# Kernel optimization log

Hardware: AMD Instinct MI355X
Metric: run time of the kernel (lower is better)

Reference implementation:

```python
import jax, jax.numpy as jnp
import numpy as np
from functools import partial

B, T, D, H, K = 4, 2048, 256, 8, 31
HD = D // H
EXP = 2  # FeedForward expansion
EPS = 1e-5


def setup_inputs() -> dict:
    key = jax.random.key(0)
    ks = iter(jax.random.split(key, 32))
    s = 0.02
    n = lambda shape: jax.random.normal(next(ks), shape, jnp.float32) * s
    ones = lambda shape: jnp.ones(shape, jnp.float32)
    zeros = lambda shape: jnp.zeros(shape, jnp.float32)
    return {
        "x": jax.random.normal(next(ks), (B, T, D), jnp.float32),
        # FF1
        "ff1_ln_g": ones((D,)), "ff1_ln_b": zeros((D,)),
        "ff1_w1": n((D, D * EXP)), "ff1_b1": zeros((D * EXP,)),
        "ff1_w2": n((D * EXP, D)), "ff1_b2": zeros((D,)),
        # MHSA
        "mhsa_ln_g": ones((D,)), "mhsa_ln_b": zeros((D,)),
        "qkv_w": n((D, 3 * D)), "qkv_b": zeros((3 * D,)),
        "out_w": n((D, D)), "out_b": zeros((D,)),
        # Conv module
        "conv_ln_g": ones((D,)), "conv_ln_b": zeros((D,)),
        "pw1_w": n((D, 2 * D)), "pw1_b": zeros((2 * D,)),
        "dw_w": n((D, 1, K)), "dw_b": zeros((D,)),
        "bn_g": ones((D,)), "bn_b": zeros((D,)),
        "pw2_w": n((D, D)), "pw2_b": zeros((D,)),
        # FF2
        "ff2_ln_g": ones((D,)), "ff2_ln_b": zeros((D,)),
        "ff2_w1": n((D, D * EXP)), "ff2_b1": zeros((D * EXP,)),
        "ff2_w2": n((D * EXP, D)), "ff2_b2": zeros((D,)),
        # Final LN
        "final_ln_g": ones((D,)), "final_ln_b": zeros((D,)),
    }


def layer_norm(x, g, b):
    mu = jnp.mean(x, axis=-1, keepdims=True)
    var = jnp.mean(jnp.square(x - mu), axis=-1, keepdims=True)
    return (x - mu) * jax.lax.rsqrt(var + EPS) * g + b


def feed_forward(x, ln_g, ln_b, w1, b1, w2, b2):
    h = layer_norm(x, ln_g, ln_b)
    h = jax.nn.silu(h @ w1 + b1)
    h = h @ w2 + b2
    return x + 0.5 * h


def mhsa(x, ln_g, ln_b, qkv_w, qkv_b, out_w, out_b):
    Bc, Tc, C = x.shape
    h = layer_norm(x, ln_g, ln_b)
    qkv = (h @ qkv_w + qkv_b).reshape(Bc, Tc, 3, H, HD)
    qkv = jnp.transpose(qkv, (2, 0, 3, 1, 4))  # [3,B,H,T,hd]
    q, k, v = qkv[0], qkv[1], qkv[2]
    attn = jnp.einsum("bhqd,bhkd->bhqk", q, k) / jnp.sqrt(jnp.float32(HD))
    attn = jax.nn.softmax(attn, axis=-1)
    out = jnp.einsum("bhqk,bhkd->bhqd", attn, v)
    out = jnp.transpose(out, (0, 2, 1, 3)).reshape(Bc, Tc, C)
    return x + (out @ out_w + out_b)


def conv_module(x, ln_g, ln_b, pw1_w, pw1_b, dw_w, dw_b, bn_g, bn_b, pw2_w, pw2_b):
    h = layer_norm(x, ln_g, ln_b)
    h = h @ pw1_w + pw1_b                      # [B,T,2D]
    a, g = jnp.split(h, 2, axis=-1)
    h = a * jax.nn.sigmoid(g)                  # GLU -> [B,T,D]
    h = jnp.transpose(h, (0, 2, 1))            # [B,D,T]
    h = jax.lax.conv_general_dilated(
        h, dw_w, window_strides=(1,), padding=[(K // 2, K // 2)],
        dimension_numbers=("NCH", "OIH", "NCH"), feature_group_count=D,
    ) + dw_b[None, :, None]
    # BatchNorm1d (training-mode batch stats, biased variance) over (B,T) per channel
    mu = jnp.mean(h, axis=(0, 2), keepdims=True)
    var = jnp.mean(jnp.square(h - mu), axis=(0, 2), keepdims=True)
    h = (h - mu) * jax.lax.rsqrt(var + EPS)
    h = h * bn_g[None, :, None] + bn_b[None, :, None]
    h = jax.nn.silu(h)
    h = jnp.transpose(h, (0, 2, 1))            # [B,T,D]
    h = h @ pw2_w + pw2_b
    return x + h


def reference(x,
              ff1_ln_g, ff1_ln_b, ff1_w1, ff1_b1, ff1_w2, ff1_b2,
              mhsa_ln_g, mhsa_ln_b, qkv_w, qkv_b, out_w, out_b,
              conv_ln_g, conv_ln_b, pw1_w, pw1_b, dw_w, dw_b, bn_g, bn_b,
              pw2_w, pw2_b,
              ff2_ln_g, ff2_ln_b, ff2_w1, ff2_b1, ff2_w2, ff2_b2,
              final_ln_g, final_ln_b):
    x = feed_forward(x, ff1_ln_g, ff1_ln_b, ff1_w1, ff1_b1, ff1_w2, ff1_b2)
    x = mhsa(x, mhsa_ln_g, mhsa_ln_b, qkv_w, qkv_b, out_w, out_b)
    x = conv_module(x, conv_ln_g, conv_ln_b, pw1_w, pw1_b, dw_w, dw_b,
                    bn_g, bn_b, pw2_w, pw2_b)
    x = feed_forward(x, ff2_ln_g, ff2_ln_b, ff2_w1, ff2_b1, ff2_w2, ff2_b2)
    return layer_norm(x, final_ln_g, final_ln_b)
```

## Files before the change

### kernel.cpp

```cpp
#include <hip/hip_runtime.h>
#include <hip/hip_bf16.h>

#define Bn 4
#define Tn 2048
#define Dn 256
#define Hn 8
#define HDn 32
#define KW 31
#define EPSV 1e-5f
#define NTOK (Bn * Tn)

typedef __attribute__((ext_vector_type(8))) short bf16x8;
typedef __attribute__((ext_vector_type(4))) float f32x4;
typedef unsigned short ushort_t;

__device__ __forceinline__ float sigmoidf_(float x) { return 1.f / (1.f + __expf(-x)); }
__device__ __forceinline__ unsigned short f2bfu(float f) {
    __hip_bfloat16 h = __float2bfloat16(f);
    unsigned short u; __builtin_memcpy(&u, &h, 2); return u;
}

template <int OUTBF>
__global__ __launch_bounds__(256) void ln_kernel(const float* __restrict__ x,
                                                 const float* __restrict__ g,
                                                 const float* __restrict__ b,
                                                 void* __restrict__ yp)
{
    const int row  = blockIdx.x * 4 + (threadIdx.x >> 6);
    const int lane = threadIdx.x & 63;
    const float* xr = x + (size_t)row * Dn + lane * 4;
    float4 v = *(const float4*)xr;
    float s = v.x + v.y + v.z + v.w;
#pragma unroll
    for (int o = 32; o > 0; o >>= 1) s += __shfl_xor(s, o, 64);
    const float mu = s * (1.f / Dn);
    const float dx = v.x - mu, dy = v.y - mu, dz = v.z - mu, dw = v.w - mu;
    float ss = dx * dx + dy * dy + dz * dz + dw * dw;
#pragma unroll
    for (int o = 32; o > 0; o >>= 1) ss += __shfl_xor(ss, o, 64);
    const float rstd = rsqrtf(ss * (1.f / Dn) + EPSV);
    const float4 gv = *(const float4*)(g + lane * 4);
    const float4 bv = *(const float4*)(b + lane * 4);
    float o0 = dx * rstd * gv.x + bv.x;
    float o1 = dy * rstd * gv.y + bv.y;
    float o2 = dz * rstd * gv.z + bv.z;
    float o3 = dw * rstd * gv.w + bv.w;
    if (OUTBF) {
        ushort4 o4;
        o4.x = f2bfu(o0); o4.y = f2bfu(o1); o4.z = f2bfu(o2); o4.w = f2bfu(o3);
        *(ushort4*)((ushort_t*)yp + (size_t)row * Dn + lane * 4) = o4;
    } else {
        float4 o4 = {o0, o1, o2, o3};
        *(float4*)((float*)yp + (size_t)row * Dn + lane * 4) = o4;
    }
}

struct WP {
    const float* s[8];
    unsigned     off[8];
    int          Kd[8];
    int          Nd[8];
};

__global__ __launch_bounds__(256) void wprep_kernel(WP p, ushort_t* __restrict__ wb)
{
    const int z = blockIdx.z;
    const int N = p.Nd[z], K = p.Kd[z];
    const int n0 = blockIdx.x * 64, k0 = blockIdx.y * 32;
    if (n0 >= N || k0 >= K) return;
    const float* src = p.s[z];
    ushort_t* dst = wb + p.off[z];
    const int nl = threadIdx.x & 63, kq = threadIdx.x >> 6;
    const int n = n0 + nl;
    const int kb = k0 + kq * 8;
    bf16x8 o;
#pragma unroll
    for (int i = 0; i < 8; ++i) o[i] = (short)f2bfu(src[(size_t)(kb + i) * N + n]);
    *(bf16x8*)(dst + (size_t)n * K + kb) = o;
}

template <int EPI, int BM>
__global__ __launch_bounds__(256) void bgemm_kernel(const ushort_t* __restrict__ A,
                                                    const ushort_t* __restrict__ Bt,
                                                    const float* __restrict__ bias,
                                                    const float* __restrict__ res,
                                                    void* __restrict__ Cp,
                                                    int N, int K, float scale)
{
    constexpr int ABLK = BM / 16;
    constexpr int AST  = ABLK / 4;
    constexpr int MT   = BM / 32;
    __shared__ ushort_t Af[ABLK][64][8];
    __shared__ ushort_t Bf[4][64][8];
    const int tid = threadIdx.x;
    const int w   = tid >> 6;
    const int l   = tid & 63;
    const int g   = l >> 4;
    const int q16 = l & 15;
    const int wm  = w >> 1;
    const int wn  = w & 1;
    const int row0 = blockIdx.x * BM;
    const int col0 = blockIdx.y * 64;
    const int sbi  = tid >> 6;

    const ushort_t* ga[AST];
#pragma unroll
    for (int i = 0; i < AST; ++i)
        ga[i] = A + (size_t)(row0 + (sbi + 4 * i) * 16 + q16) * K + g * 8;
    const ushort_t* gb = Bt + (size_t)(col0 + sbi * 16 + q16) * K + g * 8;

    f32x4 acc[MT][2];
#pragma unroll
    for (int mt = 0; mt < MT; ++mt)
#pragma unroll
        for (int nt = 0; nt < 2; ++nt) { acc[mt][nt].x = 0.f; acc[mt][nt].y = 0.f; acc[mt][nt].z = 0.f; acc[mt][nt].w = 0.f; }

    bf16x8 sa[AST], sb;
#pragma unroll
    for (int i = 0; i < AST; ++i) sa[i] = *(const bf16x8*)ga[i];
    sb = *(const bf16x8*)gb;

    const int NKT = K >> 5;
    for (int kt = 0; kt < NKT; ++kt) {
        __syncthreads();
#pragma unroll
        for (int i = 0; i < AST; ++i) *(bf16x8*)&Af[sbi + 4 * i][l][0] = sa[i];
        *(bf16x8*)&Bf[sbi][l][0] = sb;
        if (kt + 1 < NKT) {
            const int k = (kt + 1) * 32;
#pragma unroll
            for (int i = 0; i < AST; ++i) sa[i] = *(const bf16x8*)(ga[i] + k);
            sb = *(const bf16x8*)(gb + k);
        }
        __syncthreads();
        bf16x8 af[MT], bb[2];
#pragma unroll
        for (int mt = 0; mt < MT; ++mt) af[mt] = *(const bf16x8*)&Af[wm * MT + mt][l][0];
#pragma unroll
        for (int nt = 0; nt < 2; ++nt) bb[nt] = *(const bf16x8*)&Bf[wn * 2 + nt][l][0];
#pragma unroll
        for (int mt = 0; mt < MT; ++mt)
#pragma unroll
            for (int nt = 0; nt < 2; ++nt)
                acc[mt][nt] = __builtin_amdgcn_mfma_f32_16x16x32_bf16(af[mt], bb[nt], acc[mt][nt], 0, 0, 0);
    }

#pragma unroll
    for (int nt = 0; nt < 2; ++nt) {
        const int col = col0 + (wn * 2 + nt) * 16 + q16;
        const float bj = bias[col];
#pragma unroll
        for (int mt = 0; mt < MT; ++mt) {
            const int rowb = row0 + (wm * MT + mt) * 16 + g * 4;
#pragma unroll
            for (int r = 0; r < 4; ++r) {
                float v = acc[mt][nt][r] + bj;
                const size_t idx = (size_t)(rowb + r) * N + col;
                if (EPI == 1) v *= sigmoidf_(v);
                if (EPI == 0 || EPI == 1) {
                    ((ushort_t*)Cp)[idx] = f2bfu(v);
                } else if (EPI == 2) {
                    ((float*)Cp)[idx] = res[idx] + scale * v;
                } else {
                    ((float*)Cp)[idx] = v;
                }
            }
        }
    }
}

__global__ __launch_bounds__(256) void attn_mfma_kernel(const ushort_t* __restrict__ qkv,
                                                        ushort_t* __restrict__ out)
{
    __shared__ ushort_t Kl[4][64][40];
    __shared__ ushort_t Vt[4][32][72];
    __shared__ ushort_t Pl[4][16][72];

    const int tid = threadIdx.x;
    const int w   = tid >> 6;
    const int l   = tid & 63;
    const int g   = l >> 4;
    const int q16 = l & 15;
    const int b   = blockIdx.y >> 3;
    const int h   = blockIdx.y & 7;
    const int q0  = blockIdx.x * 128 + w * 32;
    const ushort_t* base = qkv + (size_t)b * Tn * 768;

    bf16x8 qf[2];
#pragma unroll
    for (int u = 0; u < 2; ++u)
        qf[u] = *(const bf16x8*)(base + (size_t)(q0 + u * 16 + q16) * 768 + h * 32 + g * 8);

    f32x4 O[2][2];
    float mrun[2][4], lrun[2][4];
#pragma unroll
    for (int u = 0; u < 2; ++u)
#pragma unroll
        for (int t = 0; t < 2; ++t) { O[u][t].x = 0.f; O[u][t].y = 0.f; O[u][t].z = 0.f; O[u][t].w = 0.f; }
#pragma unroll
    for (int u = 0; u < 2; ++u)
#pragma unroll
        for (int r = 0; r < 4; ++r) { mrun[u][r] = 0.f; lrun[u][r] = 0.f; }

    const float cs = 0.25505392367033404f;

    const ushort_t* kvp = base + (size_t)l * 768 + 256 + h * 32;
    bf16x8 nk[4], nv[4];
#pragma unroll
    for (int j = 0; j < 4; ++j) {
        nk[j] = *(const bf16x8*)(kvp + j * 8);
        nv[j] = *(const bf16x8*)(kvp + 256 + j * 8);
    }

    for (int c0 = 0; c0 < Tn; c0 += 64) {
#pragma unroll
        for (int j = 0; j < 4; ++j)
            *(bf16x8*)&Kl[w][l][j * 8] = nk[j];
#pragma unroll
        for (int j = 0; j < 4; ++j) {
            const int vcol = l ^ (16 * j);
#pragma unroll
            for (int i = 0; i < 8; ++i)
                Vt[w][j * 8 + i][vcol] = (ushort_t)nv[j][i];
        }
        if (c0 + 64 < Tn) {
            const ushort_t* np = kvp + (size_t)(c0 + 64) * 768;
#pragma unroll
            for (int j = 0; j < 4; ++j) {
                nk[j] = *(const bf16x8*)(np + j * 8);
                nv[j] = *(const bf16x8*)(np + 256 + j * 8);
            }
        }

        bf16x8 kb[4];
#pragma unroll
        for (int t = 0; t < 4; ++t)
            kb[t] = *(const bf16x8*)&Kl[w][t * 16 + q16][g * 8];
        bf16x8 vb[2][2];
#pragma unroll
        for (int ht = 0; ht < 2; ++ht) {
            const int d = ht * 16 + q16;
#pragma unroll
            for (int c = 0; c < 2; ++c)
                vb[ht][c] = *(const bf16x8*)&Vt[w][d][(c * 32 + g * 8) ^ ((d & 24) << 1)];
        }

#pragma unroll
        for (int u = 0; u < 2; ++u) {
            float p[4][4];
#pragma unroll
            for (int t = 0; t < 4; ++t) {
                f32x4 z = {0.f, 0.f, 0.f, 0.f};
                f32x4 s = __builtin_amdgcn_mfma_f32_16x16x32_bf16(qf[u], kb[t], z, 0, 0, 0);
#pragma unroll
                for (int r = 0; r < 4; ++r) p[t][r] = s[r] * cs;
            }
            float wgl = p[0][0] - mrun[u][0];
#pragma unroll
            for (int t = 0; t < 4; ++t)
#pragma unroll
                for (int r = 0; r < 4; ++r) wgl = fmaxf(wgl, p[t][r] - mrun[u][r]);
            if (__builtin_expect(__any(wgl > 11.f) != 0, 0)) {
                float mx[4];
#pragma unroll
                for (int r = 0; r < 4; ++r)
                    mx[r] = fmaxf(fmaxf(p[0][r], p[1][r]), fmaxf(p[2][r], p[3][r]));
#pragma unroll
                for (int o = 1; o < 16; o <<= 1)
#pragma unroll
                    for (int r = 0; r < 4; ++r) mx[r] = fmaxf(mx[r], __shfl_xor(mx[r], o, 64));
#pragma unroll
                for (int r = 0; r < 4; ++r) {
                    const float mn = fmaxf(mrun[u][r], mx[r]);
                    const float f  = exp2f(mrun[u][r] - mn);
                    lrun[u][r] *= f;
                    O[u][0][r] *= f;
                    O[u][1][r] *= f;
                    mrun[u][r] = mn;
                }
            }
#pragma unroll
            for (int t = 0; t < 4; ++t)
#pragma unroll
                for (int r = 0; r < 4; ++r) {
                    const float pe = exp2f(p[t][r] - mrun[u][r]);
                    lrun[u][r] += pe;
                    Pl[w][g * 4 + r][(t * 16 + q16) ^ (g << 4)] = f2bfu(pe);
                }
            bf16x8 pa[2];
#pragma unroll
            for (int c = 0; c < 2; ++c)
                pa[c] = *(const bf16x8*)&Pl[w][q16][(c * 32 + g * 8) ^ ((q16 >> 2) << 4)];
#pragma unroll
            for (int ht = 0; ht < 2; ++ht) {
                O[u][ht] = __builtin_amdgcn_mfma_f32_16x16x32_bf16(pa[0], vb[ht][0], O[u][ht], 0, 0, 0);
                O[u][ht] = __builtin_amdgcn_mfma_f32_16x16x32_bf16(pa[1], vb[ht][1], O[u][ht], 0, 0, 0);
            }
        }
    }

#pragma unroll
    for (int u = 0; u < 2; ++u) {
#pragma unroll
        for (int o = 1; o < 16; o <<= 1)
#pragma unroll
            for (int r = 0; r < 4; ++r) lrun[u][r] += __shfl_xor(lrun[u][r], o, 64);
#pragma unroll
        for (int r = 0; r < 4; ++r) {
            const float inv = 1.f / lrun[u][r];
            const int row = b * Tn + q0 + u * 16 + g * 4 + r;
#pragma unroll
            for (int ht = 0; ht < 2; ++ht)
                out[(size_t)row * Dn + h * 32 + ht * 16 + q16] = f2bfu(O[u][ht][r] * inv);
        }
    }
}

__global__ __launch_bounds__(256) void glu_kernel(const float* __restrict__ h,
                                                  float* __restrict__ outp)
{
    const size_t i   = (size_t)blockIdx.x * 256 + threadIdx.x;
    const size_t row = i / (Dn / 4);
    const int    c4  = (int)(i % (Dn / 4)) * 4;
    const float* hp  = h + row * (2 * Dn);
    const float4 a = *(const float4*)(hp + c4);
    const float4 g = *(const float4*)(hp + Dn + c4);
    float4 r;
    r.x = a.x * sigmoidf_(g.x);
    r.y = a.y * sigmoidf_(g.y);
    r.z = a.z * sigmoidf_(g.z);
    r.w = a.w * sigmoidf_(g.w);
    *(float4*)(outp + row * Dn + c4) = r;
}

__global__ __launch_bounds__(256) void dwconv_kernel(const float* __restrict__ in,
                                                     const float* __restrict__ w,
                                                     const float* __restrict__ wb,
                                                     float* __restrict__ outp)
{
    const int d  = threadIdx.x;
    const int b  = blockIdx.y;
    const int t0 = blockIdx.x * 8;
    float wr[KW];
#pragma unroll
    for (int k = 0; k < KW; ++k) wr[k] = w[d * KW + k];
    const float bias = wb[d];
    const float* bin  = in + (size_t)b * Tn * Dn + d;
    float* bout       = outp + (size_t)b * Tn * Dn + d;
    if (t0 >= (KW / 2) + 1 && t0 + 8 + KW / 2 <= Tn) {
        for (int i = 0; i < 8; ++i) {
            const int t = t0 + i;
            float s = bias;
#pragma unroll
            for (int k = 0; k < KW; ++k) s = fmaf(bin[(size_t)(t + k - KW / 2) * Dn], wr[k], s);
            bout[(size_t)t * Dn] = s;
        }
    } else {
        for (int i = 0; i < 8; ++i) {
            const int t = t0 + i;
            float s = bias;
#pragma unroll
            for (int k = 0; k < KW; ++k) {
                const int tt = t + k - KW / 2;
                if (tt >= 0 && tt < Tn) s = fmaf(bin[(size_t)tt * Dn], wr[k], s);
            }
            bout[(size_t)t * Dn] = s;
        }
    }
}

__global__ __launch_bounds__(256) void bnpart_kernel(const float* __restrict__ in,
                                                     float* __restrict__ part)
{
    const int d  = threadIdx.x;
    const int bk = blockIdx.x;
    float s = 0.f, ss = 0.f;
    const float* p = in + (size_t)bk * 32 * Dn + d;
    for (int t = 0; t < 32; ++t) {
        const float v = p[(size_t)t * Dn];
        s += v;
        ss = fmaf(v, v, ss);
    }
    part[bk * 512 + d]       = s;
    part[bk * 512 + 256 + d] = ss;
}

__global__ __launch_bounds__(256) void bnfin_kernel(const float* __restrict__ part,
                                                    float* __restrict__ meanp,
                                                    float* __restrict__ rstdp)
{
    const int d = threadIdx.x;
    float s = 0.f, ss = 0.f;
    for (int k = 0; k < 256; ++k) {
        s  += part[k * 512 + d];
        ss += part[k * 512 + 256 + d];
    }
    const float mu  = s * (1.f / NTOK);
    const float var = ss * (1.f / NTOK) - mu * mu;
    meanp[d] = mu;
    rstdp[d] = rsqrtf(var + EPSV);
}

__global__ __launch_bounds__(256) void bnsilu_kernel(const float* __restrict__ in,
                                                     const float* __restrict__ meanp,
                                                     const float* __restrict__ rstdp,
                                                     const float* __restrict__ g,
                                                     const float* __restrict__ bb,
                                                     ushort_t* __restrict__ outp)
{
    const size_t idx = ((size_t)blockIdx.x * 256 + threadIdx.x) * 4;
    const int d = (int)(idx & (Dn - 1));
    const float4 v = *(const float4*)(in + idx);
    ushort4 r;
    {
        float t;
        t = (v.x - meanp[d + 0]) * rstdp[d + 0] * g[d + 0] + bb[d + 0]; r.x = f2bfu(t * sigmoidf_(t));
        t = (v.y - meanp[d + 1]) * rstdp[d + 1] * g[d + 1] + bb[d + 1]; r.y = f2bfu(t * sigmoidf_(t));
        t = (v.z - meanp[d + 2]) * rstdp[d + 2] * g[d + 2] + bb[d + 2]; r.z = f2bfu(t * sigmoidf_(t));
        t = (v.w - meanp[d + 3]) * rstdp[d + 3] * g[d + 3] + bb[d + 3]; r.w = f2bfu(t * sigmoidf_(t));
    }
    *(ushort4*)(outp + idx) = r;
}

extern "C" void kernel_launch(void* const* d_in, const int* in_sizes, int n_in,
                              void* d_out, int out_size, void* d_ws, size_t ws_size,
                              hipStream_t stream)
{
    const float* x         = (const float*)d_in[0];
    const float* ff1_ln_g  = (const float*)d_in[1];
    const float* ff1_ln_b  = (const float*)d_in[2];
    const float* ff1_w1    = (const float*)d_in[3];
    const float* ff1_b1    = (const float*)d_in[4];
    const float* ff1_w2    = (const float*)d_in[5];
    const float* ff1_b2    = (const float*)d_in[6];
    const float* mhsa_ln_g = (const float*)d_in[7];
    const float* mhsa_ln_b = (const float*)d_in[8];
    const float* qkv_w     = (const float*)d_in[9];
    const float* qkv_b     = (const float*)d_in[10];
    const float* out_w     = (const float*)d_in[11];
    const float* out_b     = (const float*)d_in[12];
    const float* conv_ln_g = (const float*)d_in[13];
    const float* conv_ln_b = (const float*)d_in[14];
    const float* pw1_w     = (const float*)d_in[15];
    const float* pw1_b     = (const float*)d_in[16];
    const float* dw_w      = (const float*)d_in[17];
    const float* dw_b      = (const float*)d_in[18];
    const float* bn_g      = (const float*)d_in[19];
    const float* bn_b      = (const float*)d_in[20];
    const float* pw2_w     = (const float*)d_in[21];
    const float* pw2_b     = (const float*)d_in[22];
    const float* ff2_ln_g  = (const float*)d_in[23];
    const float* ff2_ln_b  = (const float*)d_in[24];
    const float* ff2_w1    = (const float*)d_in[25];
    const float* ff2_b1    = (const float*)d_in[26];
    const float* ff2_w2    = (const float*)d_in[27];
    const float* ff2_b2    = (const float*)d_in[28];
    const float* fin_ln_g  = (const float*)d_in[29];
    const float* fin_ln_b  = (const float*)d_in[30];

    char* W = (char*)d_ws;
    const size_t MB = 1u << 20;
    float*    R     = (float*)W;
    ushort_t* NbBF  = (ushort_t*)(W + 8 * MB);
    ushort_t* HBF   = (ushort_t*)(W + 12 * MB);
    float*    Hf32  = (float*)(W + 12 * MB);
    float*    Cb    = (float*)(W + 12 * MB);
    ushort_t* AtBF  = (ushort_t*)(W + 24 * MB);
    float*    part  = (float*)(W + 28 * MB);
    float*    meanp = part + 131072;
    float*    rstdp = meanp + 256;
    ushort_t* wbuf  = (ushort_t*)(W + 29 * MB);

    ushort_t* qkvT = wbuf;
    ushort_t* outT = wbuf + 196608;
    ushort_t* f11T = wbuf + 262144;
    ushort_t* f12T = wbuf + 393216;
    ushort_t* f21T = wbuf + 524288;
    ushort_t* f22T = wbuf + 655360;
    ushort_t* pw1T = wbuf + 786432;
    ushort_t* pw2T = wbuf + 917504;

    const dim3 blk(256);

    WP wp;
    wp.s[0] = qkv_w;  wp.off[0] = 0;      wp.Kd[0] = 256; wp.Nd[0] = 768;
    wp.s[1] = out_w;  wp.off[1] = 196608; wp.Kd[1] = 256; wp.Nd[1] = 256;
    wp.s[2] = ff1_w1; wp.off[2] = 262144; wp.Kd[2] = 256; wp.Nd[2] = 512;
    wp.s[3] = ff1_w2; wp.off[3] = 393216; wp.Kd[3] = 512; wp.Nd[3] = 256;
    wp.s[4] = ff2_w1; wp.off[4] = 524288; wp.Kd[4] = 256; wp.Nd[4] = 512;
    wp.s[5] = ff2_w2; wp.off[5] = 655360; wp.Kd[5] = 512; wp.Nd[5] = 256;
    wp.s[6] = pw1_w;  wp.off[6] = 786432; wp.Kd[6] = 256; wp.Nd[6] = 512;
    wp.s[7] = pw2_w;  wp.off[7] = 917504; wp.Kd[7] = 256; wp.Nd[7] = 256;
    wprep_kernel<<<dim3(12, 16, 8), blk, 0, stream>>>(wp, wbuf);

    ln_kernel<1><<<NTOK / 4, blk, 0, stream>>>(x, ff1_ln_g, ff1_ln_b, NbBF);
    bgemm_kernel<1, 128><<<dim3(64, 8), blk, 0, stream>>>(NbBF, f11T, ff1_b1, nullptr, HBF, 512, 256, 0.f);
    bgemm_kernel<2, 64><<<dim3(128, 4), blk, 0, stream>>>(HBF, f12T, ff1_b2, x, R, 256, 512, 0.5f);

    ln_kernel<1><<<NTOK / 4, blk, 0, stream>>>(R, mhsa_ln_g, mhsa_ln_b, NbBF);
    bgemm_kernel<0, 128><<<dim3(64, 12), blk, 0, stream>>>(NbBF, qkvT, qkv_b, nullptr, HBF, 768, 256, 0.f);
    attn_mfma_kernel<<<dim3(16, 32), blk, 0, stream>>>(HBF, AtBF);
    bgemm_kernel<2, 64><<<dim3(128, 4), blk, 0, stream>>>(AtBF, outT, out_b, R, R, 256, 256, 1.f);

    ln_kernel<1><<<NTOK / 4, blk, 0, stream>>>(R, conv_ln_g, conv_ln_b, NbBF);
    bgemm_kernel<3, 128><<<dim3(64, 8), blk, 0, stream>>>(NbBF, pw1T, pw1_b, nullptr, Hf32, 512, 256, 0.f);
    glu_kernel<<<NTOK * Dn / 4 / 256, blk, 0, stream>>>(Hf32, (float*)d_out);
    dwconv_kernel<<<dim3(Tn / 8, Bn), blk, 0, stream>>>((float*)d_out, dw_w, dw_b, Cb);
    bnpart_kernel<<<256, blk, 0, stream>>>(Cb, part);
    bnfin_kernel<<<1, blk, 0, stream>>>(part, meanp, rstdp);
    bnsilu_kernel<<<NTOK * Dn / 4 / 256, blk, 0, stream>>>(Cb, meanp, rstdp, bn_g, bn_b, AtBF);
    bgemm_kernel<2, 64><<<dim3(128, 4), blk, 0, stream>>>(AtBF, pw2T, pw2_b, R, R, 256, 256, 1.f);

    ln_kernel<1><<<NTOK / 4, blk, 0, stream>>>(R, ff2_ln_g, ff2_ln_b, NbBF);
    bgemm_kernel<1, 128><<<dim3(64, 8), blk, 0, stream>>>(NbBF, f21T, ff2_b1, nullptr, HBF, 512, 256, 0.f);
    bgemm_kernel<2, 64><<<dim3(128, 4), blk, 0, stream>>>(HBF, f22T, ff2_b2, R, R, 256, 512, 0.5f);

    ln_kernel<0><<<NTOK / 4, blk, 0, stream>>>(R, fin_ln_g, fin_ln_b, d_out);
}
```

Before: 369.5 us.

## Double-buffer GEMM via direct LDS loads, fuse GLU into pw1, transpose attention MFMA

The bf16 GEMM now stages A/B tiles straight into double-buffered LDS with global_load_lds, uses a 64-wide K step, and needs one barrier per iteration, so loads overlap the MFMAs. A new epilogue mode computes both GLU halves in one GEMM and writes a*sigmoid(g), which removes the fp32 pw1 intermediate and the separate GLU kernel. Attention swaps the MFMA operands so each lane owns a single query row, which cuts the per-row max and sum shuffles, and it packs P and the output with v_cvt_pk_bf16. The cost is twice the LDS per GEMM block and more accumulator registers in the GLU variant, which may reduce occupancy.

Measured after the change: 357.3 us. -3.3%, faster.

```diff
diff --git a/kernel.cpp b/kernel.cpp
--- a/kernel.cpp
+++ b/kernel.cpp
@@ -18,6 +18,15 @@
 __device__ __forceinline__ unsigned short f2bfu(float f) {
     __hip_bfloat16 h = __float2bfloat16(f);
     unsigned short u; __builtin_memcpy(&u, &h, 2); return u;
+}
+__device__ __forceinline__ unsigned cvtpk_bf16(float lo, float hi) {
+    unsigned r;
+    asm("v_cvt_pk_bf16_f32 %0, %1, %2" : "=v"(r) : "v"(lo), "v"(hi));
+    return r;
+}
+__device__ __forceinline__ void gload16(const void* g, void* l) {
+    __builtin_amdgcn_global_load_lds((const __attribute__((address_space(1))) unsigned*)g,
+                                     (__attribute__((address_space(3))) unsigned*)l, 16, 0, 0);
 }
 
 template <int OUTBF>
@@ -88,10 +97,15 @@
                                                     int N, int K, float scale)
 {
     constexpr int ABLK = BM / 16;
-    constexpr int AST  = ABLK / 4;
+    constexpr int NB   = (EPI == 4) ? 8 : 4;
+    constexpr int ASTA = ABLK * 2 / 4;
+    constexpr int ASTB = NB * 2 / 4;
     constexpr int MT   = BM / 32;
-    __shared__ ushort_t Af[ABLK][64][8];
-    __shared__ ushort_t Bf[4][64][8];
+    __shared__ ushort_t Af[2][ABLK][2][64][8];
+    __shared__ ushort_t Bf[2][NB][2][64][8];
+    constexpr int ASTRIDE = ABLK * 2 * 64 * 8;
+    constexpr int BSTRIDE = NB * 2 * 64 * 8;
+
     const int tid = threadIdx.x;
     const int w   = tid >> 6;
     const int l   = tid & 63;
@@ -101,68 +115,111 @@
     const int wn  = w & 1;
     const int row0 = blockIdx.x * BM;
     const int col0 = blockIdx.y * 64;
-    const int sbi  = tid >> 6;
-
-    const ushort_t* ga[AST];
-#pragma unroll
-    for (int i = 0; i < AST; ++i)
-        ga[i] = A + (size_t)(row0 + (sbi + 4 * i) * 16 + q16) * K + g * 8;
-    const ushort_t* gb = Bt + (size_t)(col0 + sbi * 16 + q16) * K + g * 8;
+
+    const ushort_t* gA[ASTA];
+    ushort_t* lA[ASTA];
+#pragma unroll
+    for (int i = 0; i < ASTA; ++i) {
+        const int fs = w * ASTA + i, ablk = fs >> 1, kk = fs & 1;
+        gA[i] = A + (size_t)(row0 + ablk * 16 + q16) * K + kk * 32 + g * 8;
+        lA[i] = &Af[0][ablk][kk][0][0];
+    }
+    const ushort_t* gB[ASTB];
+    ushort_t* lB[ASTB];
+#pragma unroll
+    for (int i = 0; i < ASTB; ++i) {
+        const int fs = w * ASTB + i, nblk = fs >> 1, kk = fs & 1;
+        const int coln = (EPI == 4 && nblk >= 4) ? 256 + col0 + (nblk - 4) * 16
+                                                 : col0 + nblk * 16;
+        gB[i] = Bt + (size_t)(coln + q16) * K + kk * 32 + g * 8;
+        lB[i] = &Bf[0][nblk][kk][0][0];
+    }
 
     f32x4 acc[MT][2];
 #pragma unroll
     for (int mt = 0; mt < MT; ++mt)
 #pragma unroll
         for (int nt = 0; nt < 2; ++nt) { acc[mt][nt].x = 0.f; acc[mt][nt].y = 0.f; acc[mt][nt].z = 0.f; acc[mt][nt].w = 0.f; }
-
-    bf16x8 sa[AST], sb;
-#pragma unroll
-    for (int i = 0; i < AST; ++i) sa[i] = *(const bf16x8*)ga[i];
-    sb = *(const bf16x8*)gb;
-
-    const int NKT = K >> 5;
+    f32x4 acc2[MT][2];
+    if (EPI == 4) {
+#pragma unroll
+        for (int mt = 0; mt < MT; ++mt)
+#pragma unroll
+            for (int nt = 0; nt < 2; ++nt) { acc2[mt][nt].x = 0.f; acc2[mt][nt].y = 0.f; acc2[mt][nt].z = 0.f; acc2[mt][nt].w = 0.f; }
+    }
+
+#pragma unroll
+    for (int i = 0; i < ASTA; ++i) gload16(gA[i], lA[i]);
+#pragma unroll
+    for (int i = 0; i < ASTB; ++i) gload16(gB[i], lB[i]);
+    __syncthreads();
+
+    const int NKT = K >> 6;
+    int cur = 0;
     for (int kt = 0; kt < NKT; ++kt) {
+        if (kt + 1 < NKT) {
+            const int ko = (kt + 1) * 64;
+            const int ao = (cur ^ 1) * ASTRIDE, bo = (cur ^ 1) * BSTRIDE;
+#pragma unroll
+            for (int i = 0; i < ASTA; ++i) gload16(gA[i] + ko, lA[i] + ao);
+#pragma unroll
+            for (int i = 0; i < ASTB; ++i) gload16(gB[i] + ko, lB[i] + bo);
+        }
+        bf16x8 af[2][MT], bb[2][2];
+#pragma unroll
+        for (int kk = 0; kk < 2; ++kk) {
+#pragma unroll
+            for (int mt = 0; mt < MT; ++mt) af[kk][mt] = *(const bf16x8*)&Af[cur][wm * MT + mt][kk][l][0];
+#pragma unroll
+            for (int nt = 0; nt < 2; ++nt) bb[kk][nt] = *(const bf16x8*)&Bf[cur][wn * 2 + nt][kk][l][0];
+        }
+#pragma unroll
+        for (int kk = 0; kk < 2; ++kk)
+#pragma unroll
+            for (int mt = 0; mt < MT; ++mt)
+#pragma unroll
+                for (int nt = 0; nt < 2; ++nt)
+                    acc[mt][nt] = __builtin_amdgcn_mfma_f32_16x16x32_bf16(af[kk][mt], bb[kk][nt], acc[mt][nt], 0, 0, 0);
+        if (EPI == 4) {
+            bf16x8 bg[2][2];
+#pragma unroll
+            for (int kk = 0; kk < 2; ++kk)
+#pragma unroll
+                for (int nt = 0; nt < 2; ++nt) bg[kk][nt] = *(const bf16x8*)&Bf[cur][4 + wn * 2 + nt][kk][l][0];
+#pragma unroll
+            for (int kk = 0; kk < 2; ++kk)
+#pragma unroll
+                for (int mt = 0; mt < MT; ++mt)
+#pragma unroll
+                    for (int nt = 0; nt < 2; ++nt)
+                        acc2[mt][nt] = __builtin_amdgcn_mfma_f32_16x16x32_bf16(af[kk][mt], bg[kk][nt], acc2[mt][nt], 0, 0, 0);
+        }
         __syncthreads();
-#pragma unroll
-        for (int i = 0; i < AST; ++i) *(bf16x8*)&Af[sbi + 4 * i][l][0] = sa[i];
-        *(bf16x8*)&Bf[sbi][l][0] = sb;
-        if (kt + 1 < NKT) {
-            const int k = (kt + 1) * 32;
-#pragma unroll
-            for (int i = 0; i < AST; ++i) sa[i] = *(const bf16x8*)(ga[i] + k);
-            sb = *(const bf16x8*)(gb + k);
-        }
-        __syncthreads();
-        bf16x8 af[MT], bb[2];
-#pragma unroll
-        for (int mt = 0; mt < MT; ++mt) af[mt] = *(const bf16x8*)&Af[wm * MT + mt][l][0];
-#pragma unroll
-        for (int nt = 0; nt < 2; ++nt) bb[nt] = *(const bf16x8*)&Bf[wn * 2 + nt][l][0];
-#pragma unroll
-        for (int mt = 0; mt < MT; ++mt)
-#pragma unroll
-            for (int nt = 0; nt < 2; ++nt)
-                acc[mt][nt] = __builtin_amdgcn_mfma_f32_16x16x32_bf16(af[mt], bb[nt], acc[mt][nt], 0, 0, 0);
+        cur ^= 1;
     }
 
 #pragma unroll
     for (int nt = 0; nt < 2; ++nt) {
         const int col = col0 + (wn * 2 + nt) * 16 + q16;
         const float bj = bias[col];
+        const float bj2 = (EPI == 4) ? bias[col + 256] : 0.f;
 #pragma unroll
         for (int mt = 0; mt < MT; ++mt) {
             const int rowb = row0 + (wm * MT + mt) * 16 + g * 4;
 #pragma unroll
             for (int r = 0; r < 4; ++r) {
                 float v = acc[mt][nt][r] + bj;
-                const size_t idx = (size_t)(rowb + r) * N + col;
                 if (EPI == 1) v *= sigmoidf_(v);
                 if (EPI == 0 || EPI == 1) {
-                    ((ushort_t*)Cp)[idx] = f2bfu(v);
+                    ((ushort_t*)Cp)[(size_t)(rowb + r) * N + col] = f2bfu(v);
                 } else if (EPI == 2) {
+                    const size_t idx = (size_t)(rowb + r) * N + col;
                     ((float*)Cp)[idx] = res[idx] + scale * v;
+                } else if (EPI == 3) {
+                    ((float*)Cp)[(size_t)(rowb + r) * N + col] = v;
                 } else {
-                    ((float*)Cp)[idx] = v;
+                    const float vg = acc2[mt][nt][r] + bj2;
+                    ((float*)Cp)[(size_t)(rowb + r) * 256 + col] = v * sigmoidf_(vg);
                 }
             }
         }
@@ -174,7 +231,7 @@
 {
     __shared__ ushort_t Kl[4][64][40];
     __shared__ ushort_t Vt[4][32][72];
-    __shared__ ushort_t Pl[4][16][72];
+    __shared__ unsigned P2[4][16][36];
 
     const int tid = threadIdx.x;
     const int w   = tid >> 6;
@@ -192,17 +249,19 @@
         qf[u] = *(const bf16x8*)(base + (size_t)(q0 + u * 16 + q16) * 768 + h * 32 + g * 8);
 
     f32x4 O[2][2];
-    float mrun[2][4], lrun[2][4];
-#pragma unroll
-    for (int u = 0; u < 2; ++u)
+    float mrun[2], lrun[2];
+#pragma unroll
+    for (int u = 0; u < 2; ++u) {
 #pragma unroll
         for (int t = 0; t < 2; ++t) { O[u][t].x = 0.f; O[u][t].y = 0.f; O[u][t].z = 0.f; O[u][t].w = 0.f; }
-#pragma unroll
-    for (int u = 0; u < 2; ++u)
-#pragma unroll
-        for (int r = 0; r < 4; ++r) { mrun[u][r] = 0.f; lrun[u][r] = 0.f; }
+        mrun[u] = 0.f; lrun[u] = 0.f;
+    }
 
     const float cs = 0.25505392367033404f;
+
+    unsigned* p2w  = &P2[w][0][0];
+    unsigned* p2wr = p2w + q16 * 36 + g * 2;
+    const int rdo0 = q16 * 36 + (g >> 1) * 8 + (g & 1) * 4;
 
     const ushort_t* kvp = base + (size_t)l * 768 + 256 + h * 32;
     bf16x8 nk[4], nv[4];
@@ -251,86 +310,74 @@
 #pragma unroll
             for (int t = 0; t < 4; ++t) {
                 f32x4 z = {0.f, 0.f, 0.f, 0.f};
-                f32x4 s = __builtin_amdgcn_mfma_f32_16x16x32_bf16(qf[u], kb[t], z, 0, 0, 0);
+                f32x4 s = __builtin_amdgcn_mfma_f32_16x16x32_bf16(kb[t], qf[u], z, 0, 0, 0);
 #pragma unroll
                 for (int r = 0; r < 4; ++r) p[t][r] = s[r] * cs;
             }
-            float wgl = p[0][0] - mrun[u][0];
+            float wgl = p[0][0] - mrun[u];
 #pragma unroll
             for (int t = 0; t < 4; ++t)
 #pragma unroll
-                for (int r = 0; r < 4; ++r) wgl = fmaxf(wgl, p[t][r] - mrun[u][r]);
+                for (int r = 0; r < 4; ++r) wgl = fmaxf(wgl, p[t][r] - mrun[u]);
             if (__builtin_expect(__any(wgl > 11.f) != 0, 0)) {
-                float mx[4];
-#pragma unroll
-                for (int r = 0; r < 4; ++r)
-                    mx[r] = fmaxf(fmaxf(p[0][r], p[1][r]), fmaxf(p[2][r], p[3][r]));
-#pragma unroll
-                for (int o = 1; o < 16; o <<= 1)
-#pragma unroll
-                    for (int r = 0; r < 4; ++r) mx[r] = fmaxf(mx[r], __shfl_xor(mx[r], o, 64));
+                float mx = p[0][0];
+#pragma unroll
+                for (int t = 0; t < 4; ++t)
+#pragma unroll
+                    for (int r = 0; r < 4; ++r) mx = fmaxf(mx, p[t][r]);
+                mx = fmaxf(mx, __shfl_xor(mx, 16, 64));
+                mx = fmaxf(mx, __shfl_xor(mx, 32, 64));
+                const float mn = fmaxf(mrun[u], mx);
+                const float f  = exp2f(mrun[u] - mn);
+                lrun[u] *= f;
+#pragma unroll
+                for (int ht = 0; ht < 2; ++ht)
+#pragma unroll
+                    for (int r = 0; r < 4; ++r) O[u][ht][r] *= f;
+                mrun[u] = mn;
+            }
+            float pe[4][4];
+            float ls = 0.f;
+#pragma unroll
+            for (int t = 0; t < 4; ++t)
 #pragma unroll
                 for (int r = 0; r < 4; ++r) {
-                    const float mn = fmaxf(mrun[u][r], mx[r]);
-                    const float f  = exp2f(mrun[u][r] - mn);
-                    lrun[u][r] *= f;
-                    O[u][0][r] *= f;
-                    O[u][1][r] *= f;
-                    mrun[u][r] = mn;
+                    pe[t][r] = exp2f(p[t][r] - mrun[u]);
+                    ls += pe[t][r];
                 }
-            }
-#pragma unroll
-            for (int t = 0; t < 4; ++t)
-#pragma unroll
-                for (int r = 0; r < 4; ++r) {
-                    const float pe = exp2f(p[t][r] - mrun[u][r]);
-                    lrun[u][r] += pe;
-                    Pl[w][g * 4 + r][(t * 16 + q16) ^ (g << 4)] = f2bfu(pe);
-                }
-            bf16x8 pa[2];
-#pragma unroll
-            for (int c = 0; c < 2; ++c)
-                pa[c] = *(const bf16x8*)&Pl[w][q16][(c * 32 + g * 8) ^ ((q16 >> 2) << 4)];
+            lrun[u] += ls;
+#pragma unroll
+            for (int t = 0; t < 4; ++t) {
+                uint2 wv;
+                wv.x = cvtpk_bf16(pe[t][0], pe[t][1]);
+                wv.y = cvtpk_bf16(pe[t][2], pe[t][3]);
+                *(uint2*)(p2wr + t * 8) = wv;
+            }
+            bf16x8 pb0 = *(const bf16x8*)(p2w + rdo0);
+            bf16x8 pb1 = *(const bf16x8*)(p2w + rdo0 + 16);
 #pragma unroll
             for (int ht = 0; ht < 2; ++ht) {
-                O[u][ht] = __builtin_amdgcn_mfma_f32_16x16x32_bf16(pa[0], vb[ht][0], O[u][ht], 0, 0, 0);
-                O[u][ht] = __builtin_amdgcn_mfma_f32_16x16x32_bf16(pa[1], vb[ht][1], O[u][ht], 0, 0, 0);
+                O[u][ht] = __builtin_amdgcn_mfma_f32_16x16x32_bf16(vb[ht][0], pb0, O[u][ht], 0, 0, 0);
+                O[u][ht] = __builtin_amdgcn_mfma_f32_16x16x32_bf16(vb[ht][1], pb1, O[u][ht], 0, 0, 0);
             }
         }
     }
 
 #pragma unroll
     for (int u = 0; u < 2; ++u) {
-#pragma unroll
-        for (int o = 1; o < 16; o <<= 1)
-#pragma unroll
-            for (int r = 0; r < 4; ++r) lrun[u][r] += __shfl_xor(lrun[u][r], o, 64);
-#pragma unroll
-        for (int r = 0; r < 4; ++r) {
-            const float inv = 1.f / lrun[u][r];
-            const int row = b * Tn + q0 + u * 16 + g * 4 + r;
-#pragma unroll
-            for (int ht = 0; ht < 2; ++ht)
-                out[(size_t)row * Dn + h * 32 + ht * 16 + q16] = f2bfu(O[u][ht][r] * inv);
-        }
-    }
-}
-
-__global__ __launch_bounds__(256) void glu_kernel(const float* __restrict__ h,
-                                                  float* __restrict__ outp)
-{
-    const size_t i   = (size_t)blockIdx.x * 256 + threadIdx.x;
-    const size_t row = i / (Dn / 4);
-    const int    c4  = (int)(i % (Dn / 4)) * 4;
-    const float* hp  = h + row * (2 * Dn);
-    const float4 a = *(const float4*)(hp + c4);
-    const float4 g = *(const float4*)(hp + Dn + c4);
-    float4 r;
-    r.x = a.x * sigmoidf_(g.x);
-    r.y = a.y * sigmoidf_(g.y);
-    r.z = a.z * sigmoidf_(g.z);
-    r.w = a.w * sigmoidf_(g.w);
-    *(float4*)(outp + row * Dn + c4) = r;
+        float lr = lrun[u];
+        lr += __shfl_xor(lr, 16, 64);
+        lr += __shfl_xor(lr, 32, 64);
+        const float inv = 1.f / lr;
+        const size_t row = (size_t)(b * Tn + q0 + u * 16 + q16);
+#pragma unroll
+        for (int ht = 0; ht < 2; ++ht) {
+            uint2 ov;
+            ov.x = cvtpk_bf16(O[u][ht][0] * inv, O[u][ht][1] * inv);
+            ov.y = cvtpk_bf16(O[u][ht][2] * inv, O[u][ht][3] * inv);
+            *(uint2*)(out + row * Dn + h * 32 + ht * 16 + g * 4) = ov;
+        }
+    }
 }
 
 __global__ __launch_bounds__(256) void dwconv_kernel(const float* __restrict__ in,
@@ -463,7 +510,6 @@
     float*    R     = (float*)W;
     ushort_t* NbBF  = (ushort_t*)(W + 8 * MB);
     ushort_t* HBF   = (ushort_t*)(W + 12 * MB);
-    float*    Hf32  = (float*)(W + 12 * MB);
     float*    Cb    = (float*)(W + 12 * MB);
     ushort_t* AtBF  = (ushort_t*)(W + 24 * MB);
     float*    part  = (float*)(W + 28 * MB);
@@ -503,8 +549,7 @@
     bgemm_kernel<2, 64><<<dim3(128, 4), blk, 0, stream>>>(AtBF, outT, out_b, R, R, 256, 256, 1.f);
 
     ln_kernel<1><<<NTOK / 4, blk, 0, stream>>>(R, conv_ln_g, conv_ln_b, NbBF);
-    bgemm_kernel<3, 128><<<dim3(64, 8), blk, 0, stream>>>(NbBF, pw1T, pw1_b, nullptr, Hf32, 512, 256, 0.f);
-    glu_kernel<<<NTOK * Dn / 4 / 256, blk, 0, stream>>>(Hf32, (float*)d_out);
+    bgemm_kernel<4, 64><<<dim3(128, 4), blk, 0, stream>>>(NbBF, pw1T, pw1_b, nullptr, (float*)d_out, 512, 256, 0.f);
     dwconv_kernel<<<dim3(Tn / 8, Bn), blk, 0, stream>>>((float*)d_out, dw_w, dw_b, Cb);
     bnpart_kernel<<<256, blk, 0, stream>>>(Cb, part);
     bnfin_kernel<<<1, blk, 0, stream>>>(part, meanp, rstdp);
```
